# Performance work log

Hardware: AMD Instinct MI355X
Metric: run time of the kernel (lower is better)

## Reference

```python
import jax, jax.numpy as jnp
import numpy as np

N_USER = 50000
N_ITEM = 50000
E = 600000
D = 128   # in_channels per node type
H = 128   # hidden_channels


def setup_inputs() -> dict:
    key = jax.random.key(0)
    ks = jax.random.split(key, 11)
    wscale = 1.0 / np.sqrt(D)  # stand-in for glorot
    inp = {
        "x_user": jax.random.normal(ks[0], (N_USER, D), jnp.float32),
        "x_item": jax.random.normal(ks[1], (N_ITEM, D), jnp.float32),
        "w_rates_src": jax.random.normal(ks[2], (D, H), jnp.float32) * wscale,
        "w_rates_tgt": jax.random.normal(ks[3], (D, H), jnp.float32) * wscale,
        "w_rated_src": jax.random.normal(ks[4], (D, H), jnp.float32) * wscale,
        "w_rated_tgt": jax.random.normal(ks[5], (D, H), jnp.float32) * wscale,
        "w_follows_src": jax.random.normal(ks[6], (D, H), jnp.float32) * wscale,
        "w_follows_tgt": jax.random.normal(ks[7], (D, H), jnp.float32) * wscale,
        "edge_rates": jax.random.randint(ks[8], (2, E), 0, N_ITEM, jnp.int32),
        "edge_rated": jax.random.randint(ks[9], (2, E), 0, N_USER, jnp.int32),
        "edge_follows": jax.random.randint(ks[10], (2, E), 0, N_USER, jnp.int32),
    }
    return inp


def _segment_mean(vals, idx, num_segments):
    # scatter(..., reduce='mean') into zeros: untouched rows stay 0
    s = jax.ops.segment_sum(vals, idx, num_segments=num_segments)
    cnt = jax.ops.segment_sum(jnp.ones((idx.shape[0], 1), vals.dtype), idx,
                              num_segments=num_segments)
    return s / jnp.maximum(cnt, 1.0)


def _relation(x_src, x_tgt, w_src, w_tgt, edges, n_tgt):
    src_x = x_src @ w_src                      # [N_src, H]
    tgt_x = x_tgt @ w_tgt                      # [N_tgt, H]
    msg = src_x[edges[0]]                      # gather  [E, H]
    agg = _segment_mean(msg, edges[1], n_tgt)  # scatter-mean [N_tgt, H]
    return tgt_x + agg


def reference(x_user, x_item, w_rates_src, w_rates_tgt, w_rated_src,
              w_rated_tgt, w_follows_src, w_follows_tgt, edge_rates,
              edge_rated, edge_follows):
    # ('user','rates','item') -> target item
    out_item = _relation(x_user, x_item, w_rates_src, w_rates_tgt,
                         edge_rates, N_ITEM)
    # ('item','rated_by','user') -> target user
    out_user = _relation(x_item, x_user, w_rated_src, w_rated_tgt,
                         edge_rated, N_USER)
    # ('user','follows','user') -> target user (accumulated)
    out_user = out_user + _relation(x_user, x_user, w_follows_src,
                                    w_follows_tgt, edge_follows, N_USER)
    # divide by number of relations per target type, then double relu
    out_user = jax.nn.relu(jax.nn.relu(out_user / 2.0))
    out_item = jax.nn.relu(jax.nn.relu(out_item / 1.0))
    return out_user, out_item
```

## Files before the change

kernel.cpp:

```cpp
#include <hip/hip_runtime.h>
#include <hip/hip_bf16.h>

constexpr int NN = 50000;
constexpr int DD = 128;
constexpr int EE = 600000;
constexpr long long PP = (long long)NN * DD;
constexpr int NE3 = 3 * EE;
constexpr int BPR = (NN + 63) / 64;
constexpr int NBIN = 3 * BPR;
constexpr int NB = 512;
constexpr int CH = (NE3 + NB - 1) / NB;
constexpr int CAP = 2048;
constexpr float QSCALE = 4.0f / 127.0f;

typedef __bf16 bf16x8 __attribute__((ext_vector_type(8)));
typedef float f32x4 __attribute__((ext_vector_type(4)));

__device__ inline unsigned short f2bs(float x) {
    __hip_bfloat16 b = __float2bfloat16(x);
    return *reinterpret_cast<unsigned short*>(&b);
}
__device__ inline float bs2f(unsigned short u) {
    union { float f; unsigned int u; } x; x.u = ((unsigned int)u) << 16; return x.f;
}
__device__ inline signed char q8(float x) {
    float c = fminf(fmaxf(x, -4.0f), 4.0f) * 31.75f;
    return (signed char)__float2int_rn(c);
}

__global__ void cvtx_kernel(const float* __restrict__ xu, const float* __restrict__ xi,
                            unsigned short* __restrict__ xub, unsigned short* __restrict__ xib,
                            signed char* __restrict__ xu8, signed char* __restrict__ xi8) {
    const int total = (int)(PP / 4);
    for (int i = blockIdx.x * blockDim.x + threadIdx.x; i < total;
         i += gridDim.x * blockDim.x) {
        float4 a = ((const float4*)xu)[i];
        float4 b = ((const float4*)xi)[i];
        ushort4 oa, ob;
        oa.x = f2bs(a.x); oa.y = f2bs(a.y); oa.z = f2bs(a.z); oa.w = f2bs(a.w);
        ob.x = f2bs(b.x); ob.y = f2bs(b.y); ob.z = f2bs(b.z); ob.w = f2bs(b.w);
        ((ushort4*)xub)[i] = oa;
        ((ushort4*)xib)[i] = ob;
        char4 ca, cb;
        ca.x = q8(a.x); ca.y = q8(a.y); ca.z = q8(a.z); ca.w = q8(a.w);
        cb.x = q8(b.x); cb.y = q8(b.y); cb.z = q8(b.z); cb.w = q8(b.w);
        ((char4*)xu8)[i] = ca;
        ((char4*)xi8)[i] = cb;
    }
}

__global__ void wprep_kernel(const float* __restrict__ wrt, const float* __restrict__ wft,
                             const float* __restrict__ wrs, const float* __restrict__ wfs,
                             const float* __restrict__ wit, const float* __restrict__ wis,
                             unsigned short* __restrict__ Wu, unsigned short* __restrict__ Wi) {
    int n = blockIdx.x;
    for (int k = threadIdx.x; k < 384; k += blockDim.x) {
        int seg = k >> 7, ks = k & 127;
        float v = (seg == 0) ? (wrt[ks * 128 + n] + wft[ks * 128 + n])
                : (seg == 1) ? wrs[ks * 128 + n] : wfs[ks * 128 + n];
        Wu[n * 384 + k] = f2bs(v);
    }
    for (int k = threadIdx.x; k < 256; k += blockDim.x) {
        int seg = k >> 7, ks = k & 127;
        float v = (seg == 0) ? wit[ks * 128 + n] : wis[ks * 128 + n];
        Wi[n * 256 + k] = f2bs(v);
    }
}


__global__ __launch_bounds__(256) void bucket_hist_kernel(
    const int* __restrict__ t0, const int* __restrict__ t1,
    const int* __restrict__ t2, unsigned int* __restrict__ hist) {
    __shared__ unsigned int h[NBIN];
    for (int i = threadIdx.x; i < NBIN; i += 256) h[i] = 0;
    __syncthreads();
    const int start = blockIdx.x * CH;
    const int end = (start + CH < NE3) ? start + CH : NE3;
    for (int idx = start + threadIdx.x; idx < end; idx += 256) {
        int rel = idx / EE;
        int e = idx - rel * EE;
        const int* tp = (rel == 0) ? t0 : (rel == 1) ? t1 : t2;
        atomicAdd(&h[rel * BPR + (tp[e] >> 6)], 1u);
    }
    __syncthreads();
    for (int i = threadIdx.x; i < NBIN; i += 256)
        hist[(size_t)blockIdx.x * NBIN + i] = h[i];
}

__global__ void bucket_base_kernel(const unsigned int* __restrict__ hist,
                                   unsigned int* __restrict__ base,
                                   unsigned int* __restrict__ bintot) {
    int bin = blockIdx.x * blockDim.x + threadIdx.x;
    if (bin >= NBIN) return;
    unsigned int run = 0;
    for (int b = 0; b < NB; ++b) {
        unsigned int v = hist[(size_t)b * NBIN + bin];
        base[(size_t)b * NBIN + bin] = run;
        run += v;
    }
    bintot[bin] = run;
}

__global__ __launch_bounds__(256) void scan_part_kernel(
    const int* __restrict__ cnt, int* __restrict__ rowst,
    int* __restrict__ bsum, int n) {
    const int tid = threadIdx.x;
    const int base = blockIdx.x * 4096 + tid * 16;
    int v[16];
    #pragma unroll
    for (int i = 0; i < 16; ++i) {
        int g = base + i;
        v[i] = (g < n) ? cnt[g] : 0;
    }
    int s = 0;
    #pragma unroll
    for (int i = 0; i < 16; ++i) s += v[i];
    const int lane = tid & 63, wv = tid >> 6;
    int incl = s;
    #pragma unroll
    for (int d = 1; d < 64; d <<= 1) {
        int u = __shfl_up(incl, d, 64);
        if (lane >= d) incl += u;
    }
    __shared__ int wsum[4];
    if (lane == 63) wsum[wv] = incl;
    __syncthreads();
    int woff = 0;
    for (int w = 0; w < wv; ++w) woff += wsum[w];
    int run = woff + incl - s;
    #pragma unroll
    for (int i = 0; i < 16; ++i) {
        int g = base + i;
        if (g < n) rowst[g] = run;
        run += v[i];
    }
    if (tid == 255) bsum[blockIdx.x] = woff + incl;
}

__global__ __launch_bounds__(256) void bucket_scatter_kernel(
    const int* __restrict__ s0, const int* __restrict__ t0,
    const int* __restrict__ s1, const int* __restrict__ t1,
    const int* __restrict__ s2, const int* __restrict__ t2,
    const unsigned int* __restrict__ base, const int* __restrict__ bkstart,
    unsigned int* __restrict__ bucketed) {
    __shared__ unsigned int cur[NBIN];
    for (int i = threadIdx.x; i < NBIN; i += 256)
        cur[i] = (unsigned int)bkstart[i] + base[(size_t)blockIdx.x * NBIN + i];
    __syncthreads();
    const int start = blockIdx.x * CH;
    const int end = (start + CH < NE3) ? start + CH : NE3;
    for (int idx = start + threadIdx.x; idx < end; idx += 256) {
        int rel = idx / EE;
        int e = idx - rel * EE;
        const int* tp = (rel == 0) ? t0 : (rel == 1) ? t1 : t2;
        const int* sp = (rel == 0) ? s0 : (rel == 1) ? s1 : s2;
        int t = tp[e];
        unsigned int pos = atomicAdd(&cur[rel * BPR + (t >> 6)], 1u);
        bucketed[pos] = ((unsigned int)(t & 63) << 16) | (unsigned int)sp[e];
    }
}

__global__ __launch_bounds__(256) void bucket_gather_kernel(
    const signed char* __restrict__ xu8, const signed char* __restrict__ xi8,
    const int* __restrict__ bkstart, const unsigned int* __restrict__ bucketed,
    unsigned short* __restrict__ accb) {
    __shared__ unsigned int raw[CAP];
    __shared__ unsigned short sorted[CAP];
    __shared__ unsigned int fcnt[64], fstart[64], cursor[64];

    const int b = blockIdx.x;
    const int rel = b / BPR;
    const int tb = (b - rel * BPR) * 64;
    const signed char* srcm = (rel == 0) ? xi8 : xu8;
    const int start = bkstart[b];
    const int end = (b == NBIN - 1) ? NE3 : bkstart[b + 1];

    const int tid = threadIdx.x;
    const int grp = tid >> 4;
    const int l = tid & 15;

    int s[4][8];
    int deg[4] = {0, 0, 0, 0};
    #pragma unroll
    for (int q = 0; q < 4; ++q)
        #pragma unroll
        for (int k = 0; k < 8; ++k) s[q][k] = 0;

    for (int c0 = start; c0 < end; c0 += CAP) {
        const int n = (end - c0 < CAP) ? end - c0 : CAP;
        if (tid < 64) fcnt[tid] = 0;
        __syncthreads();
        for (int i = tid; i < n; i += 256) {
            unsigned int r = bucketed[c0 + i];
            raw[i] = r;
            atomicAdd(&fcnt[r >> 16], 1u);
        }
        __syncthreads();
        if (tid < 64) {
            unsigned int v = fcnt[tid];
            unsigned int incl = v;
            #pragma unroll
            for (int d = 1; d < 64; d <<= 1) {
                unsigned int u = __shfl_up(incl, d, 64);
                if ((tid & 63) >= d) incl += u;
            }
            fstart[tid] = incl - v;
            cursor[tid] = incl - v;
        }
        __syncthreads();
        for (int i = tid; i < n; i += 256) {
            unsigned int r = raw[i];
            unsigned int pos = atomicAdd(&cursor[r >> 16], 1u);
            sorted[pos] = (unsigned short)r;
        }
        __syncthreads();

        #pragma unroll
        for (int q = 0; q < 4; ++q) {
            const int f = grp + 16 * q;
            const int cf = (int)fcnt[f];
            const int st = (int)fstart[f];
            deg[q] += cf;
            int j = 0;
            for (; j + 2 <= cf; j += 2) {
                int sa = sorted[st + j];
                int sb = sorted[st + j + 1];
                uint2 va = *(const uint2*)(srcm + (size_t)sa * DD + l * 8);
                uint2 vb = *(const uint2*)(srcm + (size_t)sb * DD + l * 8);
                #pragma unroll
                for (int k = 0; k < 4; ++k) {
                    s[q][k]     += (int)(signed char)(va.x >> (8 * k))
                                 + (int)(signed char)(vb.x >> (8 * k));
                    s[q][4 + k] += (int)(signed char)(va.y >> (8 * k))
                                 + (int)(signed char)(vb.y >> (8 * k));
                }
            }
            if (j < cf) {
                int sa = sorted[st + j];
                uint2 va = *(const uint2*)(srcm + (size_t)sa * DD + l * 8);
                #pragma unroll
                for (int k = 0; k < 4; ++k) {
                    s[q][k]     += (int)(signed char)(va.x >> (8 * k));
                    s[q][4 + k] += (int)(signed char)(va.y >> (8 * k));
                }
            }
        }
        __syncthreads();
    }

    #pragma unroll
    for (int q = 0; q < 4; ++q) {
        const int f = grp + 16 * q;
        const int t = tb + f;
        if (t < NN) {
            float inv = QSCALE / (float)(deg[q] > 1 ? deg[q] : 1);
            float m[8];
            #pragma unroll
            for (int k = 0; k < 8; ++k) m[k] = (float)s[q][k] * inv;
            uint4 o;
            o.x = ((unsigned int)f2bs(m[1]) << 16) | f2bs(m[0]);
            o.y = ((unsigned int)f2bs(m[3]) << 16) | f2bs(m[2]);
            o.z = ((unsigned int)f2bs(m[5]) << 16) | f2bs(m[4]);
            o.w = ((unsigned int)f2bs(m[7]) << 16) | f2bs(m[6]);
            *(uint4*)(accb + (size_t)(rel * NN + t) * DD + l * 8) = o;
        }
    }
}

__device__ __forceinline__ void gemm_body(
    const unsigned short* __restrict__ a0, const unsigned short* __restrict__ a1,
    const unsigned short* __restrict__ a2, const unsigned short* __restrict__ Wt,
    float* __restrict__ outp, float postmul, int ksteps,
    unsigned char* lAb, unsigned char* lBb) {
    const int tid = threadIdx.x;
    const int m0 = blockIdx.x * 128;
    const int n0 = blockIdx.y * 64;
    const int Ktot = ksteps * 64;
    const int wv = tid >> 6, lane = tid & 63;
    const int rbase = tid >> 4;
    const int ku = tid & 15;

    f32x4 acc[2][4];
    #pragma unroll
    for (int i = 0; i < 2; ++i)
        #pragma unroll
        for (int j = 0; j < 4; ++j) acc[i][j] = (f32x4)(0.f);

    unsigned long long aReg[8], bReg[4];
    {
        #pragma unroll
        for (int i = 0; i < 8; ++i) {
            int g = m0 + rbase + i * 16;
            aReg[i] = (g < NN)
                ? *(const unsigned long long*)(a0 + (size_t)g * DD + ku * 4) : 0ull;
        }
        #pragma unroll
        for (int i = 0; i < 4; ++i) {
            int n = rbase + i * 16;
            bReg[i] = *(const unsigned long long*)(Wt + (size_t)(n0 + n) * Ktot + ku * 4);
        }
    }

    for (int kt = 0; kt < ksteps; ++kt) {
        #pragma unroll
        for (int i = 0; i < 8; ++i) {
            int row = rbase + i * 16;
            int byte = (row * 128 + ku * 8) ^ ((row & 7) << 4);
            *(unsigned long long*)(lAb + byte) = aReg[i];
        }
        #pragma unroll
        for (int i = 0; i < 4; ++i) {
            int n = rbase + i * 16;
            int byte = (n * 128 + ku * 8) ^ ((n & 7) << 4);
            *(unsigned long long*)(lBb + byte) = bReg[i];
        }
        __syncthreads();

        if (kt + 1 < ksteps) {
            const int ktn = kt + 1;
            const unsigned short* As = (ktn >> 1) == 0 ? a0
                                     : (ktn >> 1) == 1 ? a1 : a2;
            const int ks0 = (ktn & 1) * 64;
            #pragma unroll
            for (int i = 0; i < 8; ++i) {
                int g = m0 + rbase + i * 16;
                aReg[i] = (g < NN)
                    ? *(const unsigned long long*)(As + (size_t)g * DD + ks0 + ku * 4)
                    : 0ull;
            }
            #pragma unroll
            for (int i = 0; i < 4; ++i) {
                int n = rbase + i * 16;
                bReg[i] = *(const unsigned long long*)(
                    Wt + (size_t)(n0 + n) * Ktot + ktn * 64 + ku * 4);
            }
        }

        #pragma unroll
        for (int kk = 0; kk < 2; ++kk) {
            bf16x8 af[2], bfr[4];
            #pragma unroll
            for (int mi = 0; mi < 2; ++mi) {
                int row = wv * 32 + mi * 16 + (lane & 15);
                int byte = (row * 128 + kk * 64 + (lane >> 4) * 16) ^ ((row & 7) << 4);
                af[mi] = *(const bf16x8*)(lAb + byte);
            }
            #pragma unroll
            for (int ni = 0; ni < 4; ++ni) {
                int n = ni * 16 + (lane & 15);
                int byte = (n * 128 + kk * 64 + (lane >> 4) * 16) ^ ((n & 7) << 4);
                bfr[ni] = *(const bf16x8*)(lBb + byte);
            }
            #pragma unroll
            for (int mi = 0; mi < 2; ++mi)
                #pragma unroll
                for (int ni = 0; ni < 4; ++ni)
                    acc[mi][ni] = __builtin_amdgcn_mfma_f32_16x16x32_bf16(
                        af[mi], bfr[ni], acc[mi][ni], 0, 0, 0);
        }
        __syncthreads();
    }

    #pragma unroll
    for (int mi = 0; mi < 2; ++mi) {
        #pragma unroll
        for (int ni = 0; ni < 4; ++ni) {
            #pragma unroll
            for (int r = 0; r < 4; ++r) {
                int g = m0 + wv * 32 + mi * 16 + (lane >> 4) * 4 + r;
                if (g < NN) {
                    float v = acc[mi][ni][r] * postmul;
                    outp[(size_t)g * DD + n0 + ni * 16 + (lane & 15)] = v > 0.f ? v : 0.f;
                }
            }
        }
    }
}

__global__ __launch_bounds__(256) void mfma_gemm2_kernel(
    const unsigned short* __restrict__ xub, const unsigned short* __restrict__ xib,
    const unsigned short* __restrict__ accb, const unsigned short* __restrict__ Wu,
    const unsigned short* __restrict__ Wi, float* __restrict__ out_user,
    float* __restrict__ out_item) {
    __shared__ unsigned char lAb[128 * 128];
    __shared__ unsigned char lBb[64 * 128];
    if (blockIdx.z == 0)
        gemm_body(xub, accb, accb + PP, Wu, out_user, 0.5f, 6, lAb, lBb);
    else
        gemm_body(xib, accb + 2 * PP, nullptr, Wi, out_item, 1.0f, 4, lAb, lBb);
}

extern "C" void kernel_launch(void* const* d_in, const int* in_sizes, int n_in,
                              void* d_out, int out_size, void* d_ws, size_t ws_size,
                              hipStream_t stream) {
    const float* x_user = (const float*)d_in[0];
    const float* x_item = (const float*)d_in[1];
    const float* w_rates_src   = (const float*)d_in[2];
    const float* w_rates_tgt   = (const float*)d_in[3];
    const float* w_rated_src   = (const float*)d_in[4];
    const float* w_rated_tgt   = (const float*)d_in[5];
    const float* w_follows_src = (const float*)d_in[6];
    const float* w_follows_tgt = (const float*)d_in[7];
    const int* e_rates   = (const int*)d_in[8];
    const int* e_rated   = (const int*)d_in[9];
    const int* e_follows = (const int*)d_in[10];

    char* p = (char*)d_ws;
    unsigned short* xub  = (unsigned short*)p; p += (size_t)PP * 2;
    unsigned short* xib  = (unsigned short*)p; p += (size_t)PP * 2;
    signed char* xu8     = (signed char*)p;   p += (size_t)PP;
    signed char* xi8     = (signed char*)p;   p += (size_t)PP;
    unsigned short* accb = (unsigned short*)p; p += (size_t)3 * PP * 2;
    unsigned short* Wu   = (unsigned short*)p; p += (size_t)128 * 384 * 2;
    unsigned short* Wi   = (unsigned short*)p; p += (size_t)128 * 256 * 2;
    unsigned int* bintot = (unsigned int*)p; p += (size_t)NBIN * 4;
    int* bkstart         = (int*)p; p += (size_t)(NBIN + 64) * 4;
    int* bsum            = (int*)p; p += (size_t)64 * 4;
    unsigned int* bucketed = (unsigned int*)p; p += (size_t)NE3 * 4;

    unsigned int* hist = (unsigned int*)accb;
    unsigned int* base = hist + (size_t)NB * NBIN;

    float* out_user = (float*)d_out;
    float* out_item = out_user + PP;

    cvtx_kernel<<<2048, 256, 0, stream>>>(x_user, x_item, xub, xib, xu8, xi8);
    wprep_kernel<<<128, 256, 0, stream>>>(w_rated_tgt, w_follows_tgt, w_rated_src,
                                          w_follows_src, w_rates_tgt, w_rates_src,
                                          Wu, Wi);
    bucket_hist_kernel<<<NB, 256, 0, stream>>>(e_rated + EE, e_follows + EE,
                                               e_rates + EE, hist);
    bucket_base_kernel<<<(NBIN + 255) / 256, 256, 0, stream>>>(hist, base, bintot);
    scan_part_kernel<<<1, 256, 0, stream>>>((const int*)bintot, bkstart, bsum, NBIN);
    bucket_scatter_kernel<<<NB, 256, 0, stream>>>(e_rated, e_rated + EE,
                                                  e_follows, e_follows + EE,
                                                  e_rates, e_rates + EE,
                                                  base, bkstart, bucketed);
    bucket_gather_kernel<<<NBIN, 256, 0, stream>>>(xu8, xi8, bkstart, bucketed, accb);

    dim3 gg((NN + 127) / 128, 2, 2);
    mfma_gemm2_kernel<<<gg, 256, 0, stream>>>(xub, xib, accb, Wu, Wi,
                                              out_user, out_item);
}
```

Measured before the change: 164.1 us.

## Widen gather to 16-byte loads and use full-width N tiles in GEMM

The bucket gather kernel now has 8 lanes per target row, each loading 16 int8 values per edge, and the inner loop is unrolled by four edges for more memory-level parallelism. The GEMM drops the split over N: each block computes all 128 output columns, so the A tile is loaded from global memory once instead of twice. The cost is more accumulator registers per thread (16 f32x4), a larger LDS B tile, and half as many blocks, which may lower occupancy.

```diff
diff --git a/kernel.cpp b/kernel.cpp
--- a/kernel.cpp
+++ b/kernel.cpp
@@ -176,15 +176,15 @@
     const int end = (b == NBIN - 1) ? NE3 : bkstart[b + 1];
 
     const int tid = threadIdx.x;
-    const int grp = tid >> 4;
-    const int l = tid & 15;
-
-    int s[4][8];
-    int deg[4] = {0, 0, 0, 0};
-    #pragma unroll
-    for (int q = 0; q < 4; ++q)
-        #pragma unroll
-        for (int k = 0; k < 8; ++k) s[q][k] = 0;
+    const int grp = tid >> 3;
+    const int l = tid & 7;
+
+    int s[2][16];
+    int deg[2] = {0, 0};
+    #pragma unroll
+    for (int q = 0; q < 2; ++q)
+        #pragma unroll
+        for (int k = 0; k < 16; ++k) s[q][k] = 0;
 
     for (int c0 = start; c0 < end; c0 += CAP) {
         const int n = (end - c0 < CAP) ? end - c0 : CAP;
@@ -216,32 +216,50 @@
         __syncthreads();
 
         #pragma unroll
-        for (int q = 0; q < 4; ++q) {
-            const int f = grp + 16 * q;
+        for (int q = 0; q < 2; ++q) {
+            const int f = grp + 32 * q;
             const int cf = (int)fcnt[f];
             const int st = (int)fstart[f];
             deg[q] += cf;
             int j = 0;
-            for (; j + 2 <= cf; j += 2) {
+            for (; j + 4 <= cf; j += 4) {
                 int sa = sorted[st + j];
                 int sb = sorted[st + j + 1];
-                uint2 va = *(const uint2*)(srcm + (size_t)sa * DD + l * 8);
-                uint2 vb = *(const uint2*)(srcm + (size_t)sb * DD + l * 8);
+                int sc = sorted[st + j + 2];
+                int sd = sorted[st + j + 3];
+                uint4 va = *(const uint4*)(srcm + (size_t)sa * DD + l * 16);
+                uint4 vb = *(const uint4*)(srcm + (size_t)sb * DD + l * 16);
+                uint4 vc = *(const uint4*)(srcm + (size_t)sc * DD + l * 16);
+                uint4 vd = *(const uint4*)(srcm + (size_t)sd * DD + l * 16);
                 #pragma unroll
                 for (int k = 0; k < 4; ++k) {
-                    s[q][k]     += (int)(signed char)(va.x >> (8 * k))
-                                 + (int)(signed char)(vb.x >> (8 * k));
-                    s[q][4 + k] += (int)(signed char)(va.y >> (8 * k))
-                                 + (int)(signed char)(vb.y >> (8 * k));
+                    s[q][k]      += (int)(signed char)(va.x >> (8 * k))
+                                  + (int)(signed char)(vb.x >> (8 * k))
+                                  + (int)(signed char)(vc.x >> (8 * k))
+                                  + (int)(signed char)(vd.x >> (8 * k));
+                    s[q][4 + k]  += (int)(signed char)(va.y >> (8 * k))
+                                  + (int)(signed char)(vb.y >> (8 * k))
+                                  + (int)(signed char)(vc.y >> (8 * k))
+                                  + (int)(signed char)(vd.y >> (8 * k));
+                    s[q][8 + k]  += (int)(signed char)(va.z >> (8 * k))
+                                  + (int)(signed char)(vb.z >> (8 * k))
+                                  + (int)(signed char)(vc.z >> (8 * k))
+                                  + (int)(signed char)(vd.z >> (8 * k));
+                    s[q][12 + k] += (int)(signed char)(va.w >> (8 * k))
+                                  + (int)(signed char)(vb.w >> (8 * k))
+                                  + (int)(signed char)(vc.w >> (8 * k))
+                                  + (int)(signed char)(vd.w >> (8 * k));
                 }
             }
-            if (j < cf) {
+            for (; j < cf; ++j) {
                 int sa = sorted[st + j];
-                uint2 va = *(const uint2*)(srcm + (size_t)sa * DD + l * 8);
+                uint4 va = *(const uint4*)(srcm + (size_t)sa * DD + l * 16);
                 #pragma unroll
                 for (int k = 0; k < 4; ++k) {
-                    s[q][k]     += (int)(signed char)(va.x >> (8 * k));
-                    s[q][4 + k] += (int)(signed char)(va.y >> (8 * k));
+                    s[q][k]      += (int)(signed char)(va.x >> (8 * k));
+                    s[q][4 + k]  += (int)(signed char)(va.y >> (8 * k));
+                    s[q][8 + k]  += (int)(signed char)(va.z >> (8 * k));
+                    s[q][12 + k] += (int)(signed char)(va.w >> (8 * k));
                 }
             }
         }
@@ -249,20 +267,26 @@
     }
 
     #pragma unroll
-    for (int q = 0; q < 4; ++q) {
-        const int f = grp + 16 * q;
+    for (int q = 0; q < 2; ++q) {
+        const int f = grp + 32 * q;
         const int t = tb + f;
         if (t < NN) {
             float inv = QSCALE / (float)(deg[q] > 1 ? deg[q] : 1);
-            float m[8];
-            #pragma unroll
-            for (int k = 0; k < 8; ++k) m[k] = (float)s[q][k] * inv;
-            uint4 o;
-            o.x = ((unsigned int)f2bs(m[1]) << 16) | f2bs(m[0]);
-            o.y = ((unsigned int)f2bs(m[3]) << 16) | f2bs(m[2]);
-            o.z = ((unsigned int)f2bs(m[5]) << 16) | f2bs(m[4]);
-            o.w = ((unsigned int)f2bs(m[7]) << 16) | f2bs(m[6]);
-            *(uint4*)(accb + (size_t)(rel * NN + t) * DD + l * 8) = o;
+            float m[16];
+            #pragma unroll
+            for (int k = 0; k < 16; ++k) m[k] = (float)s[q][k] * inv;
+            unsigned short* op = accb + (size_t)(rel * NN + t) * DD + l * 16;
+            uint4 o1, o2;
+            o1.x = ((unsigned int)f2bs(m[1]) << 16) | f2bs(m[0]);
+            o1.y = ((unsigned int)f2bs(m[3]) << 16) | f2bs(m[2]);
+            o1.z = ((unsigned int)f2bs(m[5]) << 16) | f2bs(m[4]);
+            o1.w = ((unsigned int)f2bs(m[7]) << 16) | f2bs(m[6]);
+            o2.x = ((unsigned int)f2bs(m[9]) << 16) | f2bs(m[8]);
+            o2.y = ((unsigned int)f2bs(m[11]) << 16) | f2bs(m[10]);
+            o2.z = ((unsigned int)f2bs(m[13]) << 16) | f2bs(m[12]);
+            o2.w = ((unsigned int)f2bs(m[15]) << 16) | f2bs(m[14]);
+            *(uint4*)op = o1;
+            *(uint4*)(op + 8) = o2;
         }
     }
 }
@@ -274,31 +298,25 @@
     unsigned char* lAb, unsigned char* lBb) {
     const int tid = threadIdx.x;
     const int m0 = blockIdx.x * 128;
-    const int n0 = blockIdx.y * 64;
     const int Ktot = ksteps * 64;
     const int wv = tid >> 6, lane = tid & 63;
     const int rbase = tid >> 4;
     const int ku = tid & 15;
 
-    f32x4 acc[2][4];
+    f32x4 acc[2][8];
     #pragma unroll
     for (int i = 0; i < 2; ++i)
         #pragma unroll
-        for (int j = 0; j < 4; ++j) acc[i][j] = (f32x4)(0.f);
-
-    unsigned long long aReg[8], bReg[4];
-    {
-        #pragma unroll
-        for (int i = 0; i < 8; ++i) {
-            int g = m0 + rbase + i * 16;
-            aReg[i] = (g < NN)
-                ? *(const unsigned long long*)(a0 + (size_t)g * DD + ku * 4) : 0ull;
-        }
-        #pragma unroll
-        for (int i = 0; i < 4; ++i) {
-            int n = rbase + i * 16;
-            bReg[i] = *(const unsigned long long*)(Wt + (size_t)(n0 + n) * Ktot + ku * 4);
-        }
+        for (int j = 0; j < 8; ++j) acc[i][j] = (f32x4)(0.f);
+
+    unsigned long long aReg[8], bReg[8];
+    #pragma unroll
+    for (int i = 0; i < 8; ++i) {
+        int g = m0 + rbase + i * 16;
+        aReg[i] = (g < NN)
+            ? *(const unsigned long long*)(a0 + (size_t)g * DD + ku * 4) : 0ull;
+        int n = rbase + i * 16;
+        bReg[i] = *(const unsigned long long*)(Wt + (size_t)n * Ktot + ku * 4);
     }
 
     for (int kt = 0; kt < ksteps; ++kt) {
@@ -307,11 +325,6 @@
             int row = rbase + i * 16;
             int byte = (row * 128 + ku * 8) ^ ((row & 7) << 4);
             *(unsigned long long*)(lAb + byte) = aReg[i];
-        }
-        #pragma unroll
-        for (int i = 0; i < 4; ++i) {
-            int n = rbase + i * 16;
-            int byte = (n * 128 + ku * 8) ^ ((n & 7) << 4);
             *(unsigned long long*)(lBb + byte) = bReg[i];
         }
         __syncthreads();
@@ -327,18 +340,15 @@
                 aReg[i] = (g < NN)
                     ? *(const unsigned long long*)(As + (size_t)g * DD + ks0 + ku * 4)
                     : 0ull;
-            }
-            #pragma unroll
-            for (int i = 0; i < 4; ++i) {
                 int n = rbase + i * 16;
                 bReg[i] = *(const unsigned long long*)(
-                    Wt + (size_t)(n0 + n) * Ktot + ktn * 64 + ku * 4);
+                    Wt + (size_t)n * Ktot + ktn * 64 + ku * 4);
             }
         }
 
         #pragma unroll
         for (int kk = 0; kk < 2; ++kk) {
-            bf16x8 af[2], bfr[4];
+            bf16x8 af[2];
             #pragma unroll
             for (int mi = 0; mi < 2; ++mi) {
                 int row = wv * 32 + mi * 16 + (lane & 15);
@@ -346,17 +356,15 @@
                 af[mi] = *(const bf16x8*)(lAb + byte);
             }
             #pragma unroll
-            for (int ni = 0; ni < 4; ++ni) {
+            for (int ni = 0; ni < 8; ++ni) {
                 int n = ni * 16 + (lane & 15);
                 int byte = (n * 128 + kk * 64 + (lane >> 4) * 16) ^ ((n & 7) << 4);
-                bfr[ni] = *(const bf16x8*)(lBb + byte);
-            }
-            #pragma unroll
-            for (int mi = 0; mi < 2; ++mi)
-                #pragma unroll
-                for (int ni = 0; ni < 4; ++ni)
-                    acc[mi][ni] = __builtin_amdgcn_mfma_f32_16x16x32_bf16(
-                        af[mi], bfr[ni], acc[mi][ni], 0, 0, 0);
+                bf16x8 bfr = *(const bf16x8*)(lBb + byte);
+                acc[0][ni] = __builtin_amdgcn_mfma_f32_16x16x32_bf16(
+                    af[0], bfr, acc[0][ni], 0, 0, 0);
+                acc[1][ni] = __builtin_amdgcn_mfma_f32_16x16x32_bf16(
+                    af[1], bfr, acc[1][ni], 0, 0, 0);
+            }
         }
         __syncthreads();
     }
@@ -364,13 +372,13 @@
     #pragma unroll
     for (int mi = 0; mi < 2; ++mi) {
         #pragma unroll
-        for (int ni = 0; ni < 4; ++ni) {
+        for (int ni = 0; ni < 8; ++ni) {
             #pragma unroll
             for (int r = 0; r < 4; ++r) {
                 int g = m0 + wv * 32 + mi * 16 + (lane >> 4) * 4 + r;
                 if (g < NN) {
                     float v = acc[mi][ni][r] * postmul;
-                    outp[(size_t)g * DD + n0 + ni * 16 + (lane & 15)] = v > 0.f ? v : 0.f;
+                    outp[(size_t)g * DD + ni * 16 + (lane & 15)] = v > 0.f ? v : 0.f;
                 }
             }
         }
@@ -383,8 +391,8 @@
     const unsigned short* __restrict__ Wi, float* __restrict__ out_user,
     float* __restrict__ out_item) {
     __shared__ unsigned char lAb[128 * 128];
-    __shared__ unsigned char lBb[64 * 128];
-    if (blockIdx.z == 0)
+    __shared__ unsigned char lBb[128 * 128];
+    if (blockIdx.y == 0)
         gemm_body(xub, accb, accb + PP, Wu, out_user, 0.5f, 6, lAb, lBb);
     else
         gemm_body(xib, accb + 2 * PP, nullptr, Wi, out_item, 1.0f, 4, lAb, lBb);
@@ -438,7 +446,7 @@
                                                   base, bkstart, bucketed);
     bucket_gather_kernel<<<NBIN, 256, 0, stream>>>(xu8, xi8, bkstart, bucketed, accb);
 
-    dim3 gg((NN + 127) / 128, 2, 2);
+    dim3 gg((NN + 127) / 128, 2);
     mfma_gemm2_kernel<<<gg, 256, 0, stream>>>(xub, xib, accb, Wu, Wi,
                                               out_user, out_item);
 }
```

Result: faster. 155.1 us (-5.4%).

## Use offset-uint8 SWAR accumulation in gather and full-N GEMM tiles

Applied to the files above, without the earlier changes.

The int8 quantized features are stored with a +128 offset as unsigned bytes. The gather kernel can then sum two byte lanes per 32-bit register with mask-and-add SWAR instead of per-byte sign extension, unrolling to 4 neighbours at a time and removing the bias at the end. Separately, each GEMM block now computes all 128 output columns instead of 64, which halves the A-tile loads and the grid size but doubles accumulator registers and B shared memory. The 16-bit lanes could overflow for rows with degree above roughly 256, and the larger accumulator may reduce occupancy.

```diff
diff --git a/kernel.cpp b/kernel.cpp
--- a/kernel.cpp
+++ b/kernel.cpp
@@ -23,14 +23,14 @@
 __device__ inline float bs2f(unsigned short u) {
     union { float f; unsigned int u; } x; x.u = ((unsigned int)u) << 16; return x.f;
 }
-__device__ inline signed char q8(float x) {
+__device__ inline unsigned char q8u(float x) {
     float c = fminf(fmaxf(x, -4.0f), 4.0f) * 31.75f;
-    return (signed char)__float2int_rn(c);
+    return (unsigned char)(__float2int_rn(c) + 128);
 }
 
 __global__ void cvtx_kernel(const float* __restrict__ xu, const float* __restrict__ xi,
                             unsigned short* __restrict__ xub, unsigned short* __restrict__ xib,
-                            signed char* __restrict__ xu8, signed char* __restrict__ xi8) {
+                            unsigned char* __restrict__ xu8, unsigned char* __restrict__ xi8) {
     const int total = (int)(PP / 4);
     for (int i = blockIdx.x * blockDim.x + threadIdx.x; i < total;
          i += gridDim.x * blockDim.x) {
@@ -41,11 +41,11 @@
         ob.x = f2bs(b.x); ob.y = f2bs(b.y); ob.z = f2bs(b.z); ob.w = f2bs(b.w);
         ((ushort4*)xub)[i] = oa;
         ((ushort4*)xib)[i] = ob;
-        char4 ca, cb;
-        ca.x = q8(a.x); ca.y = q8(a.y); ca.z = q8(a.z); ca.w = q8(a.w);
-        cb.x = q8(b.x); cb.y = q8(b.y); cb.z = q8(b.z); cb.w = q8(b.w);
-        ((char4*)xu8)[i] = ca;
-        ((char4*)xi8)[i] = cb;
+        uchar4 ca, cb;
+        ca.x = q8u(a.x); ca.y = q8u(a.y); ca.z = q8u(a.z); ca.w = q8u(a.w);
+        cb.x = q8u(b.x); cb.y = q8u(b.y); cb.z = q8u(b.z); cb.w = q8u(b.w);
+        ((uchar4*)xu8)[i] = ca;
+        ((uchar4*)xi8)[i] = cb;
     }
 }
 
@@ -161,7 +161,7 @@
 }
 
 __global__ __launch_bounds__(256) void bucket_gather_kernel(
-    const signed char* __restrict__ xu8, const signed char* __restrict__ xi8,
+    const unsigned char* __restrict__ xu8, const unsigned char* __restrict__ xi8,
     const int* __restrict__ bkstart, const unsigned int* __restrict__ bucketed,
     unsigned short* __restrict__ accb) {
     __shared__ unsigned int raw[CAP];
@@ -171,7 +171,7 @@
     const int b = blockIdx.x;
     const int rel = b / BPR;
     const int tb = (b - rel * BPR) * 64;
-    const signed char* srcm = (rel == 0) ? xi8 : xu8;
+    const unsigned char* srcm = (rel == 0) ? xi8 : xu8;
     const int start = bkstart[b];
     const int end = (b == NBIN - 1) ? NE3 : bkstart[b + 1];
 
@@ -179,12 +179,12 @@
     const int grp = tid >> 4;
     const int l = tid & 15;
 
-    int s[4][8];
+    unsigned int s[4][4];
     int deg[4] = {0, 0, 0, 0};
     #pragma unroll
     for (int q = 0; q < 4; ++q)
         #pragma unroll
-        for (int k = 0; k < 8; ++k) s[q][k] = 0;
+        for (int k = 0; k < 4; ++k) s[q][k] = 0u;
 
     for (int c0 = start; c0 < end; c0 += CAP) {
         const int n = (end - c0 < CAP) ? end - c0 : CAP;
@@ -222,27 +222,31 @@
             const int st = (int)fstart[f];
             deg[q] += cf;
             int j = 0;
-            for (; j + 2 <= cf; j += 2) {
+            for (; j + 4 <= cf; j += 4) {
                 int sa = sorted[st + j];
                 int sb = sorted[st + j + 1];
+                int sc = sorted[st + j + 2];
+                int sd = sorted[st + j + 3];
                 uint2 va = *(const uint2*)(srcm + (size_t)sa * DD + l * 8);
                 uint2 vb = *(const uint2*)(srcm + (size_t)sb * DD + l * 8);
-                #pragma unroll
-                for (int k = 0; k < 4; ++k) {
-                    s[q][k]     += (int)(signed char)(va.x >> (8 * k))
-                                 + (int)(signed char)(vb.x >> (8 * k));
-                    s[q][4 + k] += (int)(signed char)(va.y >> (8 * k))
-                                 + (int)(signed char)(vb.y >> (8 * k));
-                }
-            }
-            if (j < cf) {
+                uint2 vc = *(const uint2*)(srcm + (size_t)sc * DD + l * 8);
+                uint2 vd = *(const uint2*)(srcm + (size_t)sd * DD + l * 8);
+                s[q][0] += (va.x & 0x00FF00FFu) + (vb.x & 0x00FF00FFu)
+                         + (vc.x & 0x00FF00FFu) + (vd.x & 0x00FF00FFu);
+                s[q][1] += ((va.x >> 8) & 0x00FF00FFu) + ((vb.x >> 8) & 0x00FF00FFu)
+                         + ((vc.x >> 8) & 0x00FF00FFu) + ((vd.x >> 8) & 0x00FF00FFu);
+                s[q][2] += (va.y & 0x00FF00FFu) + (vb.y & 0x00FF00FFu)
+                         + (vc.y & 0x00FF00FFu) + (vd.y & 0x00FF00FFu);
+                s[q][3] += ((va.y >> 8) & 0x00FF00FFu) + ((vb.y >> 8) & 0x00FF00FFu)
+                         + ((vc.y >> 8) & 0x00FF00FFu) + ((vd.y >> 8) & 0x00FF00FFu);
+            }
+            for (; j < cf; ++j) {
                 int sa = sorted[st + j];
                 uint2 va = *(const uint2*)(srcm + (size_t)sa * DD + l * 8);
-                #pragma unroll
-                for (int k = 0; k < 4; ++k) {
-                    s[q][k]     += (int)(signed char)(va.x >> (8 * k));
-                    s[q][4 + k] += (int)(signed char)(va.y >> (8 * k));
-                }
+                s[q][0] += (va.x & 0x00FF00FFu);
+                s[q][1] += ((va.x >> 8) & 0x00FF00FFu);
+                s[q][2] += (va.y & 0x00FF00FFu);
+                s[q][3] += ((va.y >> 8) & 0x00FF00FFu);
             }
         }
         __syncthreads();
@@ -253,10 +257,17 @@
         const int f = grp + 16 * q;
         const int t = tb + f;
         if (t < NN) {
+            float bias = 128.0f * (float)deg[q];
             float inv = QSCALE / (float)(deg[q] > 1 ? deg[q] : 1);
             float m[8];
-            #pragma unroll
-            for (int k = 0; k < 8; ++k) m[k] = (float)s[q][k] * inv;
+            m[0] = ((float)(s[q][0] & 0xFFFFu) - bias) * inv;
+            m[2] = ((float)(s[q][0] >> 16)    - bias) * inv;
+            m[1] = ((float)(s[q][1] & 0xFFFFu) - bias) * inv;
+            m[3] = ((float)(s[q][1] >> 16)    - bias) * inv;
+            m[4] = ((float)(s[q][2] & 0xFFFFu) - bias) * inv;
+            m[6] = ((float)(s[q][2] >> 16)    - bias) * inv;
+            m[5] = ((float)(s[q][3] & 0xFFFFu) - bias) * inv;
+            m[7] = ((float)(s[q][3] >> 16)    - bias) * inv;
             uint4 o;
             o.x = ((unsigned int)f2bs(m[1]) << 16) | f2bs(m[0]);
             o.y = ((unsigned int)f2bs(m[3]) << 16) | f2bs(m[2]);
@@ -274,31 +285,25 @@
     unsigned char* lAb, unsigned char* lBb) {
     const int tid = threadIdx.x;
     const int m0 = blockIdx.x * 128;
-    const int n0 = blockIdx.y * 64;
     const int Ktot = ksteps * 64;
     const int wv = tid >> 6, lane = tid & 63;
     const int rbase = tid >> 4;
     const int ku = tid & 15;
 
-    f32x4 acc[2][4];
+    f32x4 acc[2][8];
     #pragma unroll
     for (int i = 0; i < 2; ++i)
         #pragma unroll
-        for (int j = 0; j < 4; ++j) acc[i][j] = (f32x4)(0.f);
-
-    unsigned long long aReg[8], bReg[4];
-    {
-        #pragma unroll
-        for (int i = 0; i < 8; ++i) {
-            int g = m0 + rbase + i * 16;
-            aReg[i] = (g < NN)
-                ? *(const unsigned long long*)(a0 + (size_t)g * DD + ku * 4) : 0ull;
-        }
-        #pragma unroll
-        for (int i = 0; i < 4; ++i) {
-            int n = rbase + i * 16;
-            bReg[i] = *(const unsigned long long*)(Wt + (size_t)(n0 + n) * Ktot + ku * 4);
-        }
+        for (int j = 0; j < 8; ++j) acc[i][j] = (f32x4)(0.f);
+
+    unsigned long long aReg[8], bReg[8];
+    #pragma unroll
+    for (int i = 0; i < 8; ++i) {
+        int g = m0 + rbase + i * 16;
+        aReg[i] = (g < NN)
+            ? *(const unsigned long long*)(a0 + (size_t)g * DD + ku * 4) : 0ull;
+        int n = rbase + i * 16;
+        bReg[i] = *(const unsigned long long*)(Wt + (size_t)n * Ktot + ku * 4);
     }
 
     for (int kt = 0; kt < ksteps; ++kt) {
@@ -307,11 +312,6 @@
             int row = rbase + i * 16;
             int byte = (row * 128 + ku * 8) ^ ((row & 7) << 4);
             *(unsigned long long*)(lAb + byte) = aReg[i];
-        }
-        #pragma unroll
-        for (int i = 0; i < 4; ++i) {
-            int n = rbase + i * 16;
-            int byte = (n * 128 + ku * 8) ^ ((n & 7) << 4);
             *(unsigned long long*)(lBb + byte) = bReg[i];
         }
         __syncthreads();
@@ -327,18 +327,15 @@
                 aReg[i] = (g < NN)
                     ? *(const unsigned long long*)(As + (size_t)g * DD + ks0 + ku * 4)
                     : 0ull;
-            }
-            #pragma unroll
-            for (int i = 0; i < 4; ++i) {
                 int n = rbase + i * 16;
                 bReg[i] = *(const unsigned long long*)(
-                    Wt + (size_t)(n0 + n) * Ktot + ktn * 64 + ku * 4);
+                    Wt + (size_t)n * Ktot + ktn * 64 + ku * 4);
             }
         }
 
         #pragma unroll
         for (int kk = 0; kk < 2; ++kk) {
-            bf16x8 af[2], bfr[4];
+            bf16x8 af[2];
             #pragma unroll
             for (int mi = 0; mi < 2; ++mi) {
                 int row = wv * 32 + mi * 16 + (lane & 15);
@@ -346,17 +343,15 @@
                 af[mi] = *(const bf16x8*)(lAb + byte);
             }
             #pragma unroll
-            for (int ni = 0; ni < 4; ++ni) {
+            for (int ni = 0; ni < 8; ++ni) {
                 int n = ni * 16 + (lane & 15);
                 int byte = (n * 128 + kk * 64 + (lane >> 4) * 16) ^ ((n & 7) << 4);
-                bfr[ni] = *(const bf16x8*)(lBb + byte);
-            }
-            #pragma unroll
-            for (int mi = 0; mi < 2; ++mi)
-                #pragma unroll
-                for (int ni = 0; ni < 4; ++ni)
-                    acc[mi][ni] = __builtin_amdgcn_mfma_f32_16x16x32_bf16(
-                        af[mi], bfr[ni], acc[mi][ni], 0, 0, 0);
+                bf16x8 bfr = *(const bf16x8*)(lBb + byte);
+                acc[0][ni] = __builtin_amdgcn_mfma_f32_16x16x32_bf16(
+                    af[0], bfr, acc[0][ni], 0, 0, 0);
+                acc[1][ni] = __builtin_amdgcn_mfma_f32_16x16x32_bf16(
+                    af[1], bfr, acc[1][ni], 0, 0, 0);
+            }
         }
         __syncthreads();
     }
@@ -364,13 +359,13 @@
     #pragma unroll
     for (int mi = 0; mi < 2; ++mi) {
         #pragma unroll
-        for (int ni = 0; ni < 4; ++ni) {
+        for (int ni = 0; ni < 8; ++ni) {
             #pragma unroll
             for (int r = 0; r < 4; ++r) {
                 int g = m0 + wv * 32 + mi * 16 + (lane >> 4) * 4 + r;
                 if (g < NN) {
                     float v = acc[mi][ni][r] * postmul;
-                    outp[(size_t)g * DD + n0 + ni * 16 + (lane & 15)] = v > 0.f ? v : 0.f;
+                    outp[(size_t)g * DD + ni * 16 + (lane & 15)] = v > 0.f ? v : 0.f;
                 }
             }
         }
@@ -383,8 +378,8 @@
     const unsigned short* __restrict__ Wi, float* __restrict__ out_user,
     float* __restrict__ out_item) {
     __shared__ unsigned char lAb[128 * 128];
-    __shared__ unsigned char lBb[64 * 128];
-    if (blockIdx.z == 0)
+    __shared__ unsigned char lBb[128 * 128];
+    if (blockIdx.y == 0)
         gemm_body(xub, accb, accb + PP, Wu, out_user, 0.5f, 6, lAb, lBb);
     else
         gemm_body(xib, accb + 2 * PP, nullptr, Wi, out_item, 1.0f, 4, lAb, lBb);
@@ -408,8 +403,8 @@
     char* p = (char*)d_ws;
     unsigned short* xub  = (unsigned short*)p; p += (size_t)PP * 2;
     unsigned short* xib  = (unsigned short*)p; p += (size_t)PP * 2;
-    signed char* xu8     = (signed char*)p;   p += (size_t)PP;
-    signed char* xi8     = (signed char*)p;   p += (size_t)PP;
+    unsigned char* xu8   = (unsigned char*)p; p += (size_t)PP;
+    unsigned char* xi8   = (unsigned char*)p; p += (size_t)PP;
     unsigned short* accb = (unsigned short*)p; p += (size_t)3 * PP * 2;
     unsigned short* Wu   = (unsigned short*)p; p += (size_t)128 * 384 * 2;
     unsigned short* Wi   = (unsigned short*)p; p += (size_t)128 * 256 * 2;
@@ -438,7 +433,7 @@
                                                   base, bkstart, bucketed);
     bucket_gather_kernel<<<NBIN, 256, 0, stream>>>(xu8, xi8, bkstart, bucketed, accb);
 
-    dim3 gg((NN + 127) / 128, 2, 2);
+    dim3 gg((NN + 127) / 128, 2);
     mfma_gemm2_kernel<<<gg, 256, 0, stream>>>(xub, xib, accb, Wu, Wi,
                                               out_user, out_item);
 }
```

New measurement: 147.2 us. -10.3%, faster.
